# Optimization experiments

Measured on AMD Instinct MI355X. Metric: run time of the kernel, lower is better.

Reference implementation:

```python
import jax, jax.numpy as jnp
import numpy as np

EPS = 0.5          # residual scaling (module __init__ eps)
N = 100_000        # num nodes
E = 1_250_000      # num edges (avg degree ~12.5)
D = 64             # feature dim


def setup_inputs() -> dict:
    key = jax.random.key(0)
    k1, k2, k3 = jax.random.split(key, 3)
    x = jax.random.normal(k1, (N, D), dtype=jnp.float32)
    src = jax.random.randint(k2, (E,), 0, N, dtype=jnp.int32)
    dst = jax.random.randint(k3, (E,), 0, N, dtype=jnp.int32)
    return {"x": x, "src": src, "dst": dst}


def reference(x, src, dst):
    n = x.shape[0]
    # out-degree of each node = number of edges with that node as source
    deg = jax.ops.segment_sum(jnp.ones(src.shape, dtype=x.dtype), src, num_segments=n)
    norm = jnp.power(jnp.maximum(deg, 1.0), -0.5)          # [N]
    edge_norm = norm[src] * norm[dst]                      # [E] (u_mul_v)
    msg = x[src] * edge_norm[:, None]                      # [E, D] (u_mul_e)
    h = jax.ops.segment_sum(msg, dst, num_segments=n)      # sum per destination
    return h + x * EPS
```

## Files before the change

kernel.cpp:

```cpp
#include <hip/hip_runtime.h>

constexpr int D        = 64;
constexpr float EPS    = 0.5f;
constexpr int BKT      = 256;
constexpr int HBKT     = 128;
constexpr int CAPB     = 4096;
constexpr int EPB      = 4096;
constexpr int PTHREADS = 512;
constexpr int EPT      = EPB / PTHREADS;
constexpr int GTHREADS = 512;
constexpr int NTHREADS = 512;
constexpr int NBMAX    = 512;
constexpr int MAXBLK   = 512;

__device__ __forceinline__ unsigned int f2bf(float f) {
    unsigned int u = __float_as_uint(f);
    return (u + 0x7FFFu + ((u >> 16) & 1u)) >> 16;
}
__device__ __forceinline__ float bf2f_lo(unsigned int v) { return __uint_as_float(v << 16); }
__device__ __forceinline__ float bf2f_hi(unsigned int v) { return __uint_as_float(v & 0xFFFF0000u); }


__global__ __launch_bounds__(PTHREADS)
void partition_kernel(const int* __restrict__ src, const int* __restrict__ dst,
                      unsigned int* __restrict__ recB, unsigned char* __restrict__ srecB,
                      unsigned short* __restrict__ tabD, unsigned short* __restrict__ tabS,
                      int E, int NB, int NBP) {
    __shared__ unsigned int  srt[EPB];
    __shared__ unsigned char ssrt[EPB];
    __shared__ unsigned int histDS[NBMAX];
    __shared__ unsigned int rsDS[NBMAX];
    __shared__ unsigned int wsums[PTHREADS / 64];
    __shared__ unsigned int carry;

    const int blk  = blockIdx.x;
    const int base = blk * EPB;
    const int tid  = threadIdx.x;
    const int lane = tid & 63;
    const int wid  = tid >> 6;
    const int cnt  = min(EPB, E - base);
    const bool full = (cnt == EPB);

    for (int b = tid; b < NB; b += PTHREADS) histDS[b] = 0;
    __syncthreads();

    if (full) {
        const int4* s4 = (const int4*)(src + base);
        const int4* d4 = (const int4*)(dst + base);
        #pragma unroll
        for (int k = 0; k < EPT / 4; ++k) {
            int4 sv = s4[tid + k * PTHREADS];
            int4 dv = d4[tid + k * PTHREADS];
            atomicAdd(&histDS[dv.x >> 8], 1u); atomicAdd(&histDS[sv.x >> 8], 0x10000u);
            atomicAdd(&histDS[dv.y >> 8], 1u); atomicAdd(&histDS[sv.y >> 8], 0x10000u);
            atomicAdd(&histDS[dv.z >> 8], 1u); atomicAdd(&histDS[sv.z >> 8], 0x10000u);
            atomicAdd(&histDS[dv.w >> 8], 1u); atomicAdd(&histDS[sv.w >> 8], 0x10000u);
        }
    } else {
        for (int k = 0; k < EPT; ++k) {
            int e = tid + k * PTHREADS;
            if (e < cnt) {
                atomicAdd(&histDS[dst[base + e] >> 8], 1u);
                atomicAdd(&histDS[src[base + e] >> 8], 0x10000u);
            }
        }
    }
    __syncthreads();

    if (tid == 0) carry = 0;
    __syncthreads();
    for (int bp = 0; bp < NB; bp += PTHREADS) {
        int idx = bp + tid;
        unsigned int orig = (idx < NB) ? histDS[idx] : 0u;
        if (idx < NB) histDS[idx] = 0;
        unsigned int v = orig;
        #pragma unroll
        for (int off = 1; off < 64; off <<= 1) {
            unsigned int t = __shfl_up(v, off);
            if (lane >= off) v += t;
        }
        if (lane == 63) wsums[wid] = v;
        __syncthreads();
        unsigned int add = carry;
        for (int w = 0; w < wid; ++w) add += wsums[w];
        if (idx < NB) rsDS[idx] = v - orig + add;
        __syncthreads();
        if (tid == 0) {
            unsigned int s = carry;
            for (int w = 0; w < PTHREADS / 64; ++w) s += wsums[w];
            carry = s;
        }
        __syncthreads();
    }

    for (int b = tid; b <= NB; b += PTHREADS) {
        unsigned int v = (b < NB) ? rsDS[b] : ((unsigned int)cnt | ((unsigned int)cnt << 16));
        tabD[(size_t)blk * NBP + b] = (unsigned short)(v & 0xFFFFu);
        tabS[(size_t)blk * NBP + b] = (unsigned short)(v >> 16);
    }

    if (full) {
        const int4* s4 = (const int4*)(src + base);
        const int4* d4 = (const int4*)(dst + base);
        #pragma unroll
        for (int k = 0; k < EPT / 4; ++k) {
            int4 sv = s4[tid + k * PTHREADS];
            int4 dv = d4[tid + k * PTHREADS];
            int ss[4] = {sv.x, sv.y, sv.z, sv.w};
            int tt[4] = {dv.x, dv.y, dv.z, dv.w};
            #pragma unroll
            for (int j = 0; j < 4; ++j) {
                int s = ss[j], t = tt[j];
                int bD = t >> 8;
                unsigned int r = atomicAdd(&histDS[bD], 1u) & 0xFFFFu;
                srt[(rsDS[bD] & 0xFFFFu) + r] = ((unsigned int)s << 8) | (unsigned int)(t & (BKT - 1));
                int bS = s >> 8;
                unsigned int r2 = atomicAdd(&histDS[bS], 0x10000u) >> 16;
                ssrt[(rsDS[bS] >> 16) + r2] = (unsigned char)(s & (BKT - 1));
            }
        }
    } else {
        for (int k = 0; k < EPT; ++k) {
            int e = tid + k * PTHREADS;
            if (e < cnt) {
                int s = src[base + e], t = dst[base + e];
                int bD = t >> 8;
                unsigned int r = atomicAdd(&histDS[bD], 1u) & 0xFFFFu;
                srt[(rsDS[bD] & 0xFFFFu) + r] = ((unsigned int)s << 8) | (unsigned int)(t & (BKT - 1));
                int bS = s >> 8;
                unsigned int r2 = atomicAdd(&histDS[bS], 0x10000u) >> 16;
                ssrt[(rsDS[bS] >> 16) + r2] = (unsigned char)(s & (BKT - 1));
            }
        }
    }
    __syncthreads();

    {
        uint4* go = (uint4*)(recB + (size_t)blk * EPB);
        const uint4* gi = (const uint4*)srt;
        for (int i = tid; i < EPB / 4; i += PTHREADS) go[i] = gi[i];
        uint4* so = (uint4*)(srecB + (size_t)blk * EPB);
        const uint4* si = (const uint4*)ssrt;
        for (int i = tid; i < EPB / 16; i += PTHREADS) so[i] = si[i];
    }
}

__global__ __launch_bounds__(NTHREADS)
void normyh_kernel(const unsigned char* __restrict__ srecB, const unsigned short* __restrict__ tabS,
                   const float2* __restrict__ x2, unsigned int* __restrict__ yh,
                   float* __restrict__ norm, int n, int NBLK, int NBP) {
    const int b   = blockIdx.x;
    const int tid = threadIdx.x;
    __shared__ unsigned int segO[MAXBLK];
    __shared__ int hist[BKT];
    __shared__ float nrm[BKT];
    if (tid < BKT) hist[tid] = 0;
    for (int blk = tid; blk < NBLK; blk += NTHREADS) {
        unsigned int o0 = tabS[(size_t)blk * NBP + b];
        unsigned int o1 = tabS[(size_t)blk * NBP + b + 1];
        segO[blk] = o0 | (o1 << 16);
    }
    __syncthreads();
    const int g  = tid >> 3;
    const int gl = tid & 7;
    for (int blk = g; blk < NBLK; blk += NTHREADS / 8) {
        unsigned int u = segO[blk];
        int o0 = (int)(u & 0xFFFFu), o1 = (int)(u >> 16);
        const unsigned char* p = srecB + (size_t)blk * EPB;
        for (int j = o0 + gl; j < o1; j += 8) atomicAdd(&hist[p[j]], 1);
    }
    __syncthreads();
    if (tid < BKT) {
        int node = b * BKT + tid;
        float nm = rsqrtf(fmaxf((float)hist[tid], 1.0f));
        nrm[tid] = nm;
        if (node < n) norm[node] = nm;
    }
    __syncthreads();
    int nodes = n - b * BKT;
    if (nodes > BKT) nodes = BKT;
    if (nodes < 0) nodes = 0;
    int total = nodes * (D / 2);
    size_t gbase = (size_t)b * BKT * (D / 2);
    for (int i = tid; i < total; i += NTHREADS) {
        float2 v = x2[gbase + i];
        float nm2 = nrm[i >> 5];
        yh[gbase + i] = f2bf(v.x * nm2) | (f2bf(v.y * nm2) << 16);
    }
}

__global__ __launch_bounds__(GTHREADS)
void sortgather_kernel(const unsigned int* __restrict__ recB, const unsigned short* __restrict__ tabD,
                       const float* __restrict__ norm, const uint4* __restrict__ yr4,
                       const float4* __restrict__ x4, float4* __restrict__ out4,
                       int n, int NBLK, int NBP) {
    __shared__ unsigned int recs[CAPB];
    __shared__ unsigned int srcs[CAPB];
    __shared__ unsigned short segoff[MAXBLK];
    __shared__ unsigned int dstoff[MAXBLK + 1];
    __shared__ int hist[HBKT];
    __shared__ int rankb[HBKT];
    __shared__ int rsL[HBKT];
    __shared__ float nrmL[HBKT];
    __shared__ unsigned int wsums[GTHREADS / 64];
    __shared__ unsigned int carry;
    const int b     = blockIdx.x >> 1;
    const int half  = blockIdx.x & 1;
    const int hbase = half * HBKT;
    const int tid   = threadIdx.x;
    const int lane  = tid & 63;
    const int wid   = tid >> 6;

    for (int blk = tid; blk < NBLK; blk += GTHREADS) {
        unsigned int o0 = tabD[(size_t)blk * NBP + b];
        unsigned int o1 = tabD[(size_t)blk * NBP + b + 1];
        segoff[blk] = (unsigned short)o0;
        dstoff[blk] = o1 - o0;
    }
    if (tid < HBKT) {
        int node = b * BKT + hbase + tid;
        nrmL[tid] = (node < n) ? norm[node] : 1.0f;
    }
    if (tid == 0) carry = 0;
    __syncthreads();
    for (int bp = 0; bp < NBLK; bp += GTHREADS) {
        int idx = bp + tid;
        unsigned int orig = (idx < NBLK) ? dstoff[idx] : 0u;
        unsigned int v = orig;
        #pragma unroll
        for (int off = 1; off < 64; off <<= 1) {
            unsigned int t = __shfl_up(v, off);
            if (lane >= off) v += t;
        }
        if (lane == 63) wsums[wid] = v;
        __syncthreads();
        unsigned int add = carry;
        for (int w = 0; w < wid; ++w) add += wsums[w];
        if (idx < NBLK) dstoff[idx] = v - orig + add;
        __syncthreads();
        if (tid == 0) {
            unsigned int s = carry;
            for (int w = 0; w < GTHREADS / 64; ++w) s += wsums[w];
            carry = s;
        }
        __syncthreads();
    }
    if (tid == 0) dstoff[NBLK] = carry;
    __syncthreads();
    const int cnt = (int)dstoff[NBLK];
    const int nch = (cnt > CAPB) ? (cnt + CAPB - 1) / CAPB : 1;

    const int fl  = lane & 7;
    const int oct = lane >> 3;

    for (int c = 0; c < nch; ++c) {
        const unsigned int lo = (unsigned int)c * CAPB;
        const unsigned int hi = min((unsigned int)cnt, lo + (unsigned int)CAPB);
        const int wlen = (int)(hi - lo);
        {
            const int cg  = tid >> 4;
            const int cgl = tid & 15;
            for (int blk = cg; blk < NBLK; blk += GTHREADS / 16) {
                unsigned int dbase = dstoff[blk], dend = dstoff[blk + 1];
                unsigned int s0 = max(dbase, lo), s1 = min(dend, hi);
                if (s0 < s1) {
                    size_t glo = (size_t)blk * EPB + segoff[blk] + (s0 - dbase);
                    for (unsigned int j = cgl; j < s1 - s0; j += 16)
                        recs[s0 - lo + j] = recB[glo + j];
                }
            }
        }
        __syncthreads();
        if (tid < HBKT) hist[tid] = 0;
        __syncthreads();
        for (int i = tid; i < wlen; i += GTHREADS) {
            int ln = (int)(recs[i] & (BKT - 1));
            if ((ln >> 7) == half) atomicAdd(&hist[ln & (HBKT - 1)], 1);
        }
        __syncthreads();
        {
            int v = (tid < HBKT) ? hist[tid] : 0;
            #pragma unroll
            for (int off = 1; off < 64; off <<= 1) {
                int t = __shfl_up(v, off);
                if (lane >= off) v += t;
            }
            if (tid < HBKT && lane == 63) wsums[wid] = (unsigned int)v;
            __syncthreads();
            if (tid < HBKT) {
                int add = (wid == 1) ? (int)wsums[0] : 0;
                int excl = v + add - hist[tid];
                rankb[tid] = excl;
                rsL[tid]   = excl;
            }
        }
        __syncthreads();
        for (int i = tid; i < wlen; i += GTHREADS) {
            unsigned int v = recs[i];
            int ln = (int)(v & (BKT - 1));
            if ((ln >> 7) == half) {
                int pos = atomicAdd(&rankb[ln & (HBKT - 1)], 1);
                srcs[pos] = v >> 8;
            }
        }
        __syncthreads();

        #pragma unroll
        for (int r = 0; r < HBKT / 64; ++r) {
            int ln   = r * 64 + wid * 8 + oct;
            int node = b * BKT + hbase + ln;
            bool valid = node < n;
            int rsl = valid ? rsL[ln]  : 0;
            int cl  = valid ? hist[ln] : 0;
            int m = cl;
            m = max(m, __shfl_xor(m, 8));
            m = max(m, __shfl_xor(m, 16));
            m = max(m, __shfl_xor(m, 32));
            float a0 = 0.f, a1 = 0.f, a2 = 0.f, a3 = 0.f;
            float a4 = 0.f, a5 = 0.f, a6 = 0.f, a7 = 0.f;
            for (int k = 0; k < m; k += 8) {
                int sb[8];
                #pragma unroll
                for (int j = 0; j < 8; ++j) {
                    int kj = k + j;
                    sb[j] = (kj < cl) ? (int)srcs[rsl + kj] : -1;
                }
                #pragma unroll
                for (int j = 0; j < 8; ++j) {
                    bool take = sb[j] >= 0;
                    int s = take ? sb[j] : 0;
                    uint4 v = yr4[(size_t)s * 8 + fl];
                    if (!take) { v.x = 0u; v.y = 0u; v.z = 0u; v.w = 0u; }
                    a0 += bf2f_lo(v.x); a1 += bf2f_hi(v.x);
                    a2 += bf2f_lo(v.y); a3 += bf2f_hi(v.y);
                    a4 += bf2f_lo(v.z); a5 += bf2f_hi(v.z);
                    a6 += bf2f_lo(v.w); a7 += bf2f_hi(v.w);
                }
            }
            if (valid) {
                float nt = nrmL[ln];
                size_t basei = (size_t)node * 16 + fl * 2;
                float4 r0, r1;
                if (c == 0) {
                    float4 xv0 = x4[basei], xv1 = x4[basei + 1];
                    r0.x = a0 * nt + EPS * xv0.x;  r0.y = a1 * nt + EPS * xv0.y;
                    r0.z = a2 * nt + EPS * xv0.z;  r0.w = a3 * nt + EPS * xv0.w;
                    r1.x = a4 * nt + EPS * xv1.x;  r1.y = a5 * nt + EPS * xv1.y;
                    r1.z = a6 * nt + EPS * xv1.z;  r1.w = a7 * nt + EPS * xv1.w;
                } else {
                    float4 p0 = out4[basei], p1 = out4[basei + 1];
                    r0.x = p0.x + a0 * nt;  r0.y = p0.y + a1 * nt;
                    r0.z = p0.z + a2 * nt;  r0.w = p0.w + a3 * nt;
                    r1.x = p1.x + a4 * nt;  r1.y = p1.y + a5 * nt;
                    r1.z = p1.z + a6 * nt;  r1.w = p1.w + a7 * nt;
                }
                out4[basei] = r0;
                out4[basei + 1] = r1;
            }
        }
    }
}


__global__ void fb_hist(const int* __restrict__ src, int* __restrict__ deg, int E) {
    int e = blockIdx.x * blockDim.x + threadIdx.x;
    if (e < E) atomicAdd(&deg[src[e]], 1);
}
__global__ void fb_norm(const int* __restrict__ deg, float* __restrict__ norm, int n) {
    int i = blockIdx.x * blockDim.x + threadIdx.x;
    if (i < n) norm[i] = rsqrtf(fmaxf((float)deg[i], 1.0f));
}
__global__ void fb_init_out(const float4* __restrict__ x, float4* __restrict__ out, int n4) {
    int i = blockIdx.x * blockDim.x + threadIdx.x;
    if (i < n4) {
        float4 v = x[i];
        out[i] = make_float4(v.x * EPS, v.y * EPS, v.z * EPS, v.w * EPS);
    }
}
__global__ void fb_scatter(const float* __restrict__ x, const int* __restrict__ src,
                           const int* __restrict__ dst, const float* __restrict__ norm,
                           float* __restrict__ out, int E) {
    long long tid = (long long)blockIdx.x * blockDim.x + threadIdx.x;
    int e = (int)(tid >> 6), d = (int)(tid & 63);
    if (e < E) {
        int s = src[e], t = dst[e];
        atomicAdd(&out[(size_t)t * D + d], norm[s] * norm[t] * x[(size_t)s * D + d]);
    }
}


extern "C" void kernel_launch(void* const* d_in, const int* in_sizes, int n_in,
                              void* d_out, int out_size, void* d_ws, size_t ws_size,
                              hipStream_t stream) {
    const float* x   = (const float*)d_in[0];
    const int*   src = (const int*)d_in[1];
    const int*   dst = (const int*)d_in[2];
    float* out = (float*)d_out;

    const int ND = in_sizes[0];
    const int E  = in_sizes[1];
    const int n  = ND / D;
    const int NB   = (n + BKT - 1) / BKT;
    const int NBLK = (E + EPB - 1) / EPB;
    const int NBP  = NB + 1;
    constexpr int B = 256;

    size_t off = 0;
    auto take = [&](size_t bytes) { size_t o = off; off = (off + bytes + 15) & ~15ull; return o; };
    size_t o_rec  = take((size_t)NBLK * EPB * 4);
    size_t o_srec = take((size_t)NBLK * EPB);
    size_t o_tabD = take((size_t)NBLK * NBP * 2);
    size_t o_tabS = take((size_t)NBLK * NBP * 2);
    size_t o_yh   = take((size_t)ND * 2);
    size_t o_norm = take((size_t)n * 4);
    size_t need = off;

    if (NB <= NBMAX && NBLK <= MAXBLK && n < (1 << 24) && need <= ws_size && E > 0) {
        char* ws = (char*)d_ws;
        unsigned int*   recB  = (unsigned int*)(ws + o_rec);
        unsigned char*  srecB = (unsigned char*)(ws + o_srec);
        unsigned short* tabD  = (unsigned short*)(ws + o_tabD);
        unsigned short* tabS  = (unsigned short*)(ws + o_tabS);
        unsigned int*   yh    = (unsigned int*)(ws + o_yh);
        float*          norm  = (float*)(ws + o_norm);

        partition_kernel<<<NBLK, PTHREADS, 0, stream>>>(src, dst, recB, srecB,
                                                        tabD, tabS, E, NB, NBP);
        normyh_kernel<<<NB, NTHREADS, 0, stream>>>(srecB, tabS, (const float2*)x, yh, norm,
                                                   n, NBLK, NBP);
        sortgather_kernel<<<2 * NB, GTHREADS, 0, stream>>>(recB, tabD, norm, (const uint4*)yh,
                                                           (const float4*)x, (float4*)out,
                                                           n, NBLK, NBP);
    } else {
        int*   deg  = (int*)d_ws;
        float* norm = (float*)d_ws + n;
        hipMemsetAsync(deg, 0, (size_t)n * sizeof(int), stream);
        fb_hist<<<(E + B - 1) / B, B, 0, stream>>>(src, deg, E);
        fb_norm<<<(n + B - 1) / B, B, 0, stream>>>(deg, norm, n);
        fb_init_out<<<(ND / 4 + B - 1) / B, B, 0, stream>>>((const float4*)x, (float4*)out, ND / 4);
        long long total = (long long)E * D;
        fb_scatter<<<(int)((total + B - 1) / B), B, 0, stream>>>(x, src, dst, norm, out, E);
    }
}
```

Measured before the change: 169.9 us.

## Shrink partition blocks, split degree-norm from bf16 conversion, drop half-bucket gather split

Partition blocks now handle 2048 edges with 256 threads, which doubles the number of partition blocks (MAXBLK raised to 1024). The degree/norm computation is split into its own kernel, and the bf16 scaled-feature conversion moves to a separate grid-stride kernel so that work is no longer tied to one block per bucket. The sort-gather kernel now handles a full 256-node bucket per block instead of two half-bucket blocks. This removes the duplicated record loading and filtering each half-block did, at the cost of fewer gather blocks, more segments to scan per bucket, an extra kernel launch, and a smaller chunk capacity that may force more chunks.

After: 166.6 us. Within noise of the previous version (-2.0%).

```diff
diff --git a/kernel.cpp b/kernel.cpp
--- a/kernel.cpp
+++ b/kernel.cpp
@@ -3,15 +3,13 @@
 constexpr int D        = 64;
 constexpr float EPS    = 0.5f;
 constexpr int BKT      = 256;
-constexpr int HBKT     = 128;
-constexpr int CAPB     = 4096;
-constexpr int EPB      = 4096;
-constexpr int PTHREADS = 512;
+constexpr int CAPB     = 3584;
+constexpr int EPB      = 2048;
+constexpr int PTHREADS = 256;
 constexpr int EPT      = EPB / PTHREADS;
 constexpr int GTHREADS = 512;
-constexpr int NTHREADS = 512;
 constexpr int NBMAX    = 512;
-constexpr int MAXBLK   = 512;
+constexpr int MAXBLK   = 1024;
 
 __device__ __forceinline__ unsigned int f2bf(float f) {
     unsigned int u = __float_as_uint(f);
@@ -145,17 +143,15 @@
     }
 }
 
-__global__ __launch_bounds__(NTHREADS)
-void normyh_kernel(const unsigned char* __restrict__ srecB, const unsigned short* __restrict__ tabS,
-                   const float2* __restrict__ x2, unsigned int* __restrict__ yh,
-                   float* __restrict__ norm, int n, int NBLK, int NBP) {
+__global__ __launch_bounds__(256)
+void degnorm_kernel(const unsigned char* __restrict__ srecB, const unsigned short* __restrict__ tabS,
+                    float* __restrict__ norm, int n, int NBLK, int NBP) {
     const int b   = blockIdx.x;
     const int tid = threadIdx.x;
     __shared__ unsigned int segO[MAXBLK];
     __shared__ int hist[BKT];
-    __shared__ float nrm[BKT];
-    if (tid < BKT) hist[tid] = 0;
-    for (int blk = tid; blk < NBLK; blk += NTHREADS) {
+    hist[tid] = 0;
+    for (int blk = tid; blk < NBLK; blk += 256) {
         unsigned int o0 = tabS[(size_t)blk * NBP + b];
         unsigned int o1 = tabS[(size_t)blk * NBP + b + 1];
         segO[blk] = o0 | (o1 << 16);
@@ -163,29 +159,25 @@
     __syncthreads();
     const int g  = tid >> 3;
     const int gl = tid & 7;
-    for (int blk = g; blk < NBLK; blk += NTHREADS / 8) {
+    for (int blk = g; blk < NBLK; blk += 32) {
         unsigned int u = segO[blk];
         int o0 = (int)(u & 0xFFFFu), o1 = (int)(u >> 16);
         const unsigned char* p = srecB + (size_t)blk * EPB;
         for (int j = o0 + gl; j < o1; j += 8) atomicAdd(&hist[p[j]], 1);
     }
     __syncthreads();
-    if (tid < BKT) {
-        int node = b * BKT + tid;
-        float nm = rsqrtf(fmaxf((float)hist[tid], 1.0f));
-        nrm[tid] = nm;
-        if (node < n) norm[node] = nm;
-    }
-    __syncthreads();
-    int nodes = n - b * BKT;
-    if (nodes > BKT) nodes = BKT;
-    if (nodes < 0) nodes = 0;
-    int total = nodes * (D / 2);
-    size_t gbase = (size_t)b * BKT * (D / 2);
-    for (int i = tid; i < total; i += NTHREADS) {
-        float2 v = x2[gbase + i];
-        float nm2 = nrm[i >> 5];
-        yh[gbase + i] = f2bf(v.x * nm2) | (f2bf(v.y * nm2) << 16);
+    int node = b * BKT + tid;
+    if (node < n) norm[node] = rsqrtf(fmaxf((float)hist[tid], 1.0f));
+}
+
+__global__ __launch_bounds__(256)
+void yhconv_kernel(const float2* __restrict__ x2, const float* __restrict__ norm,
+                   unsigned int* __restrict__ yh, int total) {
+    int stride = gridDim.x * 256;
+    for (int i = blockIdx.x * 256 + threadIdx.x; i < total; i += stride) {
+        float2 v = x2[i];
+        float nm = norm[i >> 5];
+        yh[i] = f2bf(v.x * nm) | (f2bf(v.y * nm) << 16);
     }
 }
 
@@ -198,18 +190,16 @@
     __shared__ unsigned int srcs[CAPB];
     __shared__ unsigned short segoff[MAXBLK];
     __shared__ unsigned int dstoff[MAXBLK + 1];
-    __shared__ int hist[HBKT];
-    __shared__ int rankb[HBKT];
-    __shared__ int rsL[HBKT];
-    __shared__ float nrmL[HBKT];
+    __shared__ int hist[BKT];
+    __shared__ int rankb[BKT];
+    __shared__ int rsL[BKT];
+    __shared__ float nrmL[BKT];
     __shared__ unsigned int wsums[GTHREADS / 64];
     __shared__ unsigned int carry;
-    const int b     = blockIdx.x >> 1;
-    const int half  = blockIdx.x & 1;
-    const int hbase = half * HBKT;
-    const int tid   = threadIdx.x;
-    const int lane  = tid & 63;
-    const int wid   = tid >> 6;
+    const int b    = blockIdx.x;
+    const int tid  = threadIdx.x;
+    const int lane = tid & 63;
+    const int wid  = tid >> 6;
 
     for (int blk = tid; blk < NBLK; blk += GTHREADS) {
         unsigned int o0 = tabD[(size_t)blk * NBP + b];
@@ -217,8 +207,8 @@
         segoff[blk] = (unsigned short)o0;
         dstoff[blk] = o1 - o0;
     }
-    if (tid < HBKT) {
-        int node = b * BKT + hbase + tid;
+    if (tid < BKT) {
+        int node = b * BKT + tid;
         nrmL[tid] = (node < n) ? norm[node] : 1.0f;
     }
     if (tid == 0) carry = 0;
@@ -258,37 +248,35 @@
         const unsigned int hi = min((unsigned int)cnt, lo + (unsigned int)CAPB);
         const int wlen = (int)(hi - lo);
         {
-            const int cg  = tid >> 4;
-            const int cgl = tid & 15;
-            for (int blk = cg; blk < NBLK; blk += GTHREADS / 16) {
+            const int cg  = tid >> 3;
+            const int cgl = tid & 7;
+            for (int blk = cg; blk < NBLK; blk += GTHREADS / 8) {
                 unsigned int dbase = dstoff[blk], dend = dstoff[blk + 1];
                 unsigned int s0 = max(dbase, lo), s1 = min(dend, hi);
                 if (s0 < s1) {
                     size_t glo = (size_t)blk * EPB + segoff[blk] + (s0 - dbase);
-                    for (unsigned int j = cgl; j < s1 - s0; j += 16)
+                    for (unsigned int j = cgl; j < s1 - s0; j += 8)
                         recs[s0 - lo + j] = recB[glo + j];
                 }
             }
         }
         __syncthreads();
-        if (tid < HBKT) hist[tid] = 0;
-        __syncthreads();
-        for (int i = tid; i < wlen; i += GTHREADS) {
-            int ln = (int)(recs[i] & (BKT - 1));
-            if ((ln >> 7) == half) atomicAdd(&hist[ln & (HBKT - 1)], 1);
-        }
+        if (tid < BKT) hist[tid] = 0;
+        __syncthreads();
+        for (int i = tid; i < wlen; i += GTHREADS) atomicAdd(&hist[recs[i] & (BKT - 1)], 1);
         __syncthreads();
         {
-            int v = (tid < HBKT) ? hist[tid] : 0;
+            int v = (tid < BKT) ? hist[tid] : 0;
             #pragma unroll
             for (int off = 1; off < 64; off <<= 1) {
                 int t = __shfl_up(v, off);
                 if (lane >= off) v += t;
             }
-            if (tid < HBKT && lane == 63) wsums[wid] = (unsigned int)v;
+            if (tid < BKT && lane == 63) wsums[wid] = (unsigned int)v;
             __syncthreads();
-            if (tid < HBKT) {
-                int add = (wid == 1) ? (int)wsums[0] : 0;
+            if (tid < BKT) {
+                int add = 0;
+                for (int w = 0; w < wid; ++w) add += (int)wsums[w];
                 int excl = v + add - hist[tid];
                 rankb[tid] = excl;
                 rsL[tid]   = excl;
@@ -297,18 +285,15 @@
         __syncthreads();
         for (int i = tid; i < wlen; i += GTHREADS) {
             unsigned int v = recs[i];
-            int ln = (int)(v & (BKT - 1));
-            if ((ln >> 7) == half) {
-                int pos = atomicAdd(&rankb[ln & (HBKT - 1)], 1);
-                srcs[pos] = v >> 8;
-            }
+            int pos = atomicAdd(&rankb[v & (BKT - 1)], 1);
+            srcs[pos] = v >> 8;
         }
         __syncthreads();
 
         #pragma unroll
-        for (int r = 0; r < HBKT / 64; ++r) {
+        for (int r = 0; r < BKT / 64; ++r) {
             int ln   = r * 64 + wid * 8 + oct;
-            int node = b * BKT + hbase + ln;
+            int node = b * BKT + ln;
             bool valid = node < n;
             int rsl = valid ? rsL[ln]  : 0;
             int cl  = valid ? hist[ln] : 0;
@@ -426,11 +411,13 @@
 
         partition_kernel<<<NBLK, PTHREADS, 0, stream>>>(src, dst, recB, srecB,
                                                         tabD, tabS, E, NB, NBP);
-        normyh_kernel<<<NB, NTHREADS, 0, stream>>>(srecB, tabS, (const float2*)x, yh, norm,
-                                                   n, NBLK, NBP);
-        sortgather_kernel<<<2 * NB, GTHREADS, 0, stream>>>(recB, tabD, norm, (const uint4*)yh,
-                                                           (const float4*)x, (float4*)out,
-                                                           n, NBLK, NBP);
+        degnorm_kernel<<<NB, 256, 0, stream>>>(srecB, tabS, norm, n, NBLK, NBP);
+        int yt = ND / 2;
+        int yg = (yt + 255) / 256; if (yg > 2048) yg = 2048;
+        yhconv_kernel<<<yg, 256, 0, stream>>>((const float2*)x, norm, yh, yt);
+        sortgather_kernel<<<NB, GTHREADS, 0, stream>>>(recB, tabD, norm, (const uint4*)yh,
+                                                       (const float4*)x, (float4*)out,
+                                                       n, NBLK, NBP);
     } else {
         int*   deg  = (int*)d_ws;
         float* norm = (float*)d_ws + n;
```
